# Kernel optimization log

Measured on AMD Instinct MI355X. Metric: run time of the kernel, lower is better.

## Reference

```python
import jax, jax.numpy as jnp
import numpy as np
from jax import lax

EPS = 1e-5

def _conv(x, w, stride=1, pad=0, groups=1):
    return lax.conv_general_dilated(
        x, w, (stride, stride), ((pad, pad), (pad, pad)),
        dimension_numbers=('NCHW', 'OIHW', 'NCHW'),
        feature_group_count=groups)

def _bn(x, gamma, beta):
    # BatchNorm2d, training-mode batch statistics (biased variance)
    mean = jnp.mean(x, axis=(0, 2, 3), keepdims=True)
    var = jnp.var(x, axis=(0, 2, 3), keepdims=True)
    xn = (x - mean) * lax.rsqrt(var + EPS)
    return xn * gamma[None, :, None, None] + beta[None, :, None, None]

def _silu(x):
    return x * jax.nn.sigmoid(x)

def setup_inputs() -> dict:
    key = jax.random.key(0)
    ks = jax.random.split(key, 20)
    B, C, H, W = 16, 128, 128, 128
    L2 = 100
    s = 0.05
    d = {
        'x': jax.random.normal(ks[0], (B, C, H, W), jnp.float32),
        'dce_output': jax.random.normal(ks[1], (B, L2, C), jnp.float32),
        # per-channel 3x3 convs fused as one depthwise conv [C,1,3,3]
        'dw_conv': jax.random.normal(ks[2], (C, 1, 3, 3), jnp.float32) * s,
        'W_dce1': jax.random.normal(ks[3], (L2 * C, C), jnp.float32) * s,
        'b_dce1': jnp.zeros((C,), jnp.float32),
        'W_dce2': jax.random.normal(ks[4], (C, C), jnp.float32) * s,
        'b_dce2': jnp.zeros((C,), jnp.float32),
        'W_sh': jax.random.normal(ks[5], (C, C // 2), jnp.float32) * s,
        'b_sh': jnp.zeros((C // 2,), jnp.float32),
        'W_ex': jax.random.normal(ks[6], (C // 2, C), jnp.float32) * s,
        'b_ex': jnp.zeros((C,), jnp.float32),
        'conv1_w': jax.random.normal(ks[7], (C, C, 3, 3), jnp.float32) * s,
        'bn1_g': jnp.ones((C,), jnp.float32),
        'bn1_b': jnp.zeros((C,), jnp.float32),
        'conv2_w': jax.random.normal(ks[8], (C, C, 1, 1), jnp.float32) * s,
        'bn2_g': jnp.ones((C,), jnp.float32),
        'bn2_b': jnp.zeros((C,), jnp.float32),
        'sc_w': jax.random.normal(ks[9], (C, C, 1, 1), jnp.float32) * s,
        'bnsc_g': jnp.ones((C,), jnp.float32),
        'bnsc_b': jnp.zeros((C,), jnp.float32),
    }
    return d

def reference(x, dce_output, dw_conv, W_dce1, b_dce1, W_dce2, b_dce2,
              W_sh, b_sh, W_ex, b_ex, conv1_w, bn1_g, bn1_b,
              conv2_w, bn2_g, bn2_b, sc_w, bnsc_g, bnsc_b):
    B, C, H, W = x.shape
    stride = 1
    # DCE FFN: Linear -> GELU(exact) -> Linear
    dce_flat = dce_output.reshape(B, -1)
    h = jax.nn.gelu(dce_flat @ W_dce1 + b_dce1, approximate=False)
    dce_features = h @ W_dce2 + b_dce2  # [B, C]
    # per-channel 3x3 conv + global avg pool, fused as depthwise conv
    sp = _conv(x, dw_conv, stride=1, pad=1, groups=C)
    spatial_features = jnp.mean(sp, axis=(2, 3))  # [B, C]
    # SE-style modulation
    m = dce_features * spatial_features
    shrunk = jax.nn.gelu(m @ W_sh + b_sh, approximate=False)
    mod_w = jax.nn.sigmoid(shrunk @ W_ex + b_ex)  # [B, C]
    xm = x * mod_w[:, :, None, None]
    # ResBlock
    bb = _bn(_conv(xm, conv1_w, stride=stride, pad=1), bn1_g, bn1_b)
    bb = _silu(bb)
    bb = _bn(_conv(bb, conv2_w, stride=1, pad=0), bn2_g, bn2_b)
    sc = _bn(_conv(xm, sc_w, stride=stride, pad=0), bnsc_g, bnsc_b)
    return _silu(bb + sc)
```

## Files before the change

### kernel.cpp

```cpp
#include <hip/hip_runtime.h>
#include <hip/hip_bf16.h>

typedef _Float16 f16;
typedef __attribute__((ext_vector_type(8))) _Float16 f16x8;
typedef __attribute__((ext_vector_type(4))) float f32x4;

__device__ __forceinline__ float geluf(float x) {
    return 0.5f * x * (1.0f + erff(x * 0.70710678118654752440f));
}
__device__ __forceinline__ float sigmf(float x) { return 1.0f / (1.0f + __expf(-x)); }

#define NB 16
#define NC 128
#define NH 128
#define NW 128
#define PLANE (NH * NW)
#define NSTAT 262144.0f

__device__ __align__(16) f16 g_Wc[9 * 4 * 128 * 32];
__device__ __align__(16) f16 g_Wsc[4 * 128 * 32];
__device__ __align__(16) f16 g_W2[4 * 128 * 32];
__device__ __align__(16) f16 g_xmT[(size_t)16 * 128 * 4 * 130 * 32];

__global__ __launch_bounds__(256) void k_wprep(const float* __restrict__ c1w,
                                               const float* __restrict__ scw,
                                               const float* __restrict__ c2w) {
    int i = blockIdx.x * 256 + threadIdx.x;
    if (i < 147456) {
        int tap = i / 16384;
        int rem = i - tap * 16384;
        int chunk = rem >> 12;
        int r2 = rem & 4095;
        int co = r2 >> 5;
        int cil = r2 & 31;
        int ci = chunk * 32 + cil;
        g_Wc[i] = (f16)c1w[((size_t)co * 128 + ci) * 9 + tap];
    } else if (i < 163840) {
        int j = i - 147456;
        int chunk = j >> 12;
        int r2 = j & 4095;
        int co = r2 >> 5;
        int cil = r2 & 31;
        g_Wsc[j] = (f16)scw[(size_t)co * 128 + chunk * 32 + cil];
    } else if (i < 180224) {
        int j = i - 163840;
        int chunk = j >> 12;
        int r2 = j & 4095;
        int co = r2 >> 5;
        int cil = j & 31;
        g_W2[j] = (f16)c2w[(size_t)co * 128 + chunk * 32 + cil];
    }
}

__global__ __launch_bounds__(256) void k_dce1(const float* __restrict__ dce,
                                              const float* __restrict__ W1,
                                              const float* __restrict__ b1,
                                              float* __restrict__ out_h) {
    int b = blockIdx.x;
    int t = threadIdx.x;
    int j = t & 127;
    int half = t >> 7;
    __shared__ float sdce[12800];
    __shared__ float sred[256];
    const float* drow = dce + (size_t)b * 12800;
    for (int i = t; i < 3200; i += 256) {
        float4 v = *(const float4*)&drow[i * 4];
        *(float4*)&sdce[i * 4] = v;
    }
    __syncthreads();
    float acc = 0.0f;
    int k0 = half * 6400;
    const float* Wp = W1 + (size_t)k0 * 128 + j;
    for (int k = 0; k < 6400; ++k) acc += sdce[k0 + k] * Wp[(size_t)k * 128];
    sred[t] = acc;
    __syncthreads();
    if (t < 128) {
        float v = sred[t] + sred[t + 128] + b1[j];
        out_h[b * 128 + j] = geluf(v);
    }
}

__global__ __launch_bounds__(128) void k_dce2(const float* __restrict__ h,
                                              const float* __restrict__ W2,
                                              const float* __restrict__ b2,
                                              float* __restrict__ feat) {
    int b = blockIdx.x, j = threadIdx.x;
    __shared__ float sh[128];
    sh[j] = h[b * 128 + j];
    __syncthreads();
    float acc = b2[j];
    for (int k = 0; k < 128; ++k) acc += sh[k] * W2[k * 128 + j];
    feat[b * 128 + j] = acc;
}

__global__ __launch_bounds__(256) void k_spatial(const float* __restrict__ x,
                                                 const float* __restrict__ dw,
                                                 float* __restrict__ spat) {
    int bc = blockIdx.x;
    int t = threadIdx.x;
    const float* p = x + (size_t)bc * PLANE;
    float f = 0, r0 = 0, r1 = 0, c0 = 0, c1 = 0;
    for (int i = t; i < PLANE; i += 256) {
        float v = p[i];
        int row = i >> 7, col = i & 127;
        f += v;
        if (row == 0) r0 += v;
        if (row == 127) r1 += v;
        if (col == 0) c0 += v;
        if (col == 127) c1 += v;
    }
    __shared__ float s[256];
    __shared__ float red[5];
    float vals[5] = {f, r0, r1, c0, c1};
    for (int k = 0; k < 5; ++k) {
        s[t] = vals[k];
        __syncthreads();
        for (int o = 128; o > 0; o >>= 1) {
            if (t < o) s[t] += s[t + o];
            __syncthreads();
        }
        if (t == 0) red[k] = s[0];
        __syncthreads();
    }
    if (t == 0) {
        int c = bc & 127;
        float full = red[0], row0 = red[1], row127 = red[2], col0 = red[3], col127 = red[4];
        float x00 = p[0];
        float x0e = p[127];
        float xe0 = p[127 * 128];
        float xee = p[127 * 128 + 127];
        float acc = 0.0f;
        for (int kh = 0; kh < 3; ++kh)
            for (int kw = 0; kw < 3; ++kw) {
                int dh = kh - 1, dwv = kw - 1;
                float T = full;
                if (dh == -1) T -= row127;
                else if (dh == 1) T -= row0;
                if (dwv == -1) T -= col127;
                else if (dwv == 1) T -= col0;
                if (dh == -1 && dwv == -1) T += xee;
                if (dh == -1 && dwv == 1) T += xe0;
                if (dh == 1 && dwv == -1) T += x0e;
                if (dh == 1 && dwv == 1) T += x00;
                acc += dw[c * 9 + kh * 3 + kw] * T;
            }
        spat[bc] = acc * (1.0f / 16384.0f);
    }
}

__global__ __launch_bounds__(128) void k_mod(const float* __restrict__ feat,
                                             const float* __restrict__ spat,
                                             const float* __restrict__ Wsh,
                                             const float* __restrict__ bsh,
                                             const float* __restrict__ Wex,
                                             const float* __restrict__ bex,
                                             float* __restrict__ mod) {
    int b = blockIdx.x, t = threadIdx.x;
    __shared__ float sm[128], ssh[64];
    sm[t] = feat[b * 128 + t] * spat[b * 128 + t];
    __syncthreads();
    if (t < 64) {
        float acc = bsh[t];
        for (int c = 0; c < 128; ++c) acc += sm[c] * Wsh[c * 64 + t];
        ssh[t] = geluf(acc);
    }
    __syncthreads();
    float acc = bex[t];
    for (int k = 0; k < 64; ++k) acc += ssh[k] * Wex[k * 128 + t];
    mod[b * 128 + t] = sigmf(acc);
}

__global__ __launch_bounds__(256) void k_xprep(const float* __restrict__ x,
                                               const float* __restrict__ mod) {
    int bid = blockIdx.x;
    int h = bid & 127;
    int b = bid >> 7;
    int t = threadIdx.x;
    __shared__ float sx[32][133];

    for (int chunk = 0; chunk < 4; ++chunk) {
        __syncthreads();
#pragma unroll
        for (int it = 0; it < 4; ++it) {
            int ci = it * 8 + (t >> 5);
            int w4 = t & 31;
            int cig = chunk * 32 + ci;
            float4 v = *(const float4*)&x[(((size_t)b * 128 + cig) * 128 + h) * 128 + w4 * 4];
            float m = mod[b * 128 + cig];
            sx[ci][w4 * 4 + 0] = v.x * m;
            sx[ci][w4 * 4 + 1] = v.y * m;
            sx[ci][w4 * 4 + 2] = v.z * m;
            sx[ci][w4 * 4 + 3] = v.w * m;
        }
        __syncthreads();
        f16* dstc = g_xmT + (((size_t)(b * 128 + h)) * 4 + chunk) * 4160;
        for (int g = t; g < 520; g += 256) {
            int s = g >> 2, c8 = g & 3;
            f16x8 o;
            if (s == 0 || s == 129) {
#pragma unroll
                for (int j = 0; j < 8; ++j) o[j] = (f16)0.f;
            } else {
#pragma unroll
                for (int j = 0; j < 8; ++j) o[j] = (f16)sx[c8 * 8 + j][s - 1];
            }
            *(f16x8*)(dstc + s * 32 + c8 * 8) = o;
        }
    }
}

__global__ __launch_bounds__(256, 2) void k_conv1m(float* __restrict__ y1,
                                                   float* __restrict__ stats) {
    int bid = blockIdx.x;
    int h = bid & 127;
    int b = bid >> 7;
    int t = threadIdx.x;
    int lane = t & 63;
    int wv = t >> 6;
    int l15 = lane & 15, lg = lane >> 4;
    int co_half = (wv >> 1) * 64;
    int w_half = (wv & 1) * 64;

    __shared__ f16 xs[3][130][40];

    f32x4 acc[4][4], asc[4][4];
#pragma unroll
    for (int ct = 0; ct < 4; ++ct)
#pragma unroll
        for (int wt = 0; wt < 4; ++wt) {
            acc[ct][wt] = (f32x4){0.f, 0.f, 0.f, 0.f};
            asc[ct][wt] = (f32x4){0.f, 0.f, 0.f, 0.f};
        }

    f16x8 z8;
#pragma unroll
    for (int j = 0; j < 8; ++j) z8[j] = (f16)0.f;

    for (int chunk = 0; chunk < 4; ++chunk) {
        __syncthreads();
        for (int g = t; g < 1560; g += 256) {
            int r = g / 520;
            int q = g - r * 520;
            int s = q >> 2, c8 = q & 3;
            int hr = h + r - 1;
            f16x8 v = z8;
            if ((unsigned)hr < 128u)
                v = *(const f16x8*)(g_xmT + (((size_t)(b * 128 + hr)) * 4 + chunk) * 4160 + s * 32 + c8 * 8);
            *(f16x8*)&xs[r][s][c8 * 8] = v;
        }
        __syncthreads();

#pragma unroll
        for (int tap = 0; tap < 9; ++tap) {
            const int kh = tap / 3, kw = tap - kh * 3;
            f16x8 af[4], bf[4];
#pragma unroll
            for (int ct = 0; ct < 4; ++ct)
                af[ct] = *(const f16x8*)(g_Wc + ((size_t)(tap * 4 + chunk) * 128 + co_half + ct * 16 + l15) * 32 + lg * 8);
#pragma unroll
            for (int wt = 0; wt < 4; ++wt)
                bf[wt] = *(const f16x8*)&xs[kh][w_half + wt * 16 + l15 + kw][lg * 8];
#pragma unroll
            for (int ct = 0; ct < 4; ++ct)
#pragma unroll
                for (int wt = 0; wt < 4; ++wt)
                    acc[ct][wt] = __builtin_amdgcn_mfma_f32_16x16x32_f16(
                        af[ct], bf[wt], acc[ct][wt], 0, 0, 0);

            if (tap == 4) {
                f16x8 sf[4];
#pragma unroll
                for (int ct = 0; ct < 4; ++ct)
                    sf[ct] = *(const f16x8*)(g_Wsc + ((size_t)chunk * 128 + co_half + ct * 16 + l15) * 32 + lg * 8);
#pragma unroll
                for (int ct = 0; ct < 4; ++ct)
#pragma unroll
                    for (int wt = 0; wt < 4; ++wt)
                        asc[ct][wt] = __builtin_amdgcn_mfma_f32_16x16x32_f16(
                            sf[ct], bf[wt], asc[ct][wt], 0, 0, 0);
            }
        }
    }

    float* yb = y1 + (size_t)b * 128 * PLANE + (size_t)h * 128;
#pragma unroll
    for (int ct = 0; ct < 4; ++ct) {
#pragma unroll
        for (int r = 0; r < 4; ++r) {
            int co = co_half + ct * 16 + lg * 4 + r;
            float s = 0, q = 0, ss = 0, qq = 0;
#pragma unroll
            for (int wt = 0; wt < 4; ++wt) {
                float v = acc[ct][wt][r];
                yb[(size_t)co * PLANE + w_half + wt * 16 + l15] = v;
                s += v; q += v * v;
                float u = asc[ct][wt][r];
                ss += u; qq += u * u;
            }
#pragma unroll
            for (int o = 1; o < 16; o <<= 1) {
                s += __shfl_xor(s, o);
                q += __shfl_xor(q, o);
                ss += __shfl_xor(ss, o);
                qq += __shfl_xor(qq, o);
            }
            if (l15 == 0) {
                atomicAdd(&stats[co], s);
                atomicAdd(&stats[128 + co], q);
                atomicAdd(&stats[256 + co], ss);
                atomicAdd(&stats[384 + co], qq);
            }
        }
    }
}

__global__ __launch_bounds__(256) void k_fin1(const float* __restrict__ stats,
                                              const float* __restrict__ g1, const float* __restrict__ be1,
                                              const float* __restrict__ gsc, const float* __restrict__ bsc,
                                              float* __restrict__ coef) {
    int t = threadIdx.x;
    const float inv = 1.0f / NSTAT;
    if (t < 128) {
        float m = stats[t] * inv;
        float v = stats[128 + t] * inv - m * m;
        float a = g1[t] * rsqrtf(v + 1e-5f);
        coef[t] = a;
        coef[128 + t] = be1[t] - m * a;
    } else {
        int c = t - 128;
        float m = stats[256 + c] * inv;
        float v = stats[384 + c] * inv - m * m;
        float a = gsc[c] * rsqrtf(v + 1e-5f);
        coef[256 + c] = a;
        coef[384 + c] = bsc[c] - m * a;
    }
}

__global__ __launch_bounds__(256, 2) void k_conv2m(const float* __restrict__ y1,
                                                   const float* __restrict__ coef,
                                                   float* __restrict__ stats) {
    int bid = blockIdx.x;
    int h = bid & 127;
    int b = bid >> 7;
    int t = threadIdx.x;
    int lane = t & 63;
    int wv = t >> 6;
    int l15 = lane & 15, lg = lane >> 4;
    int co_half = (wv >> 1) * 64;
    int w_half = (wv & 1) * 64;

    __shared__ float sy[32][133];
    __shared__ f16 bbs[128][40];

    f32x4 acc[4][4];
#pragma unroll
    for (int ct = 0; ct < 4; ++ct)
#pragma unroll
        for (int wt = 0; wt < 4; ++wt) acc[ct][wt] = (f32x4){0.f, 0.f, 0.f, 0.f};

    for (int chunk = 0; chunk < 4; ++chunk) {
        __syncthreads();
#pragma unroll
        for (int it = 0; it < 4; ++it) {
            int ci = it * 8 + (t >> 5);
            int w4 = t & 31;
            int cig = chunk * 32 + ci;
            float a = coef[cig], c = coef[128 + cig];
            float4 v = *(const float4*)&y1[(((size_t)b * 128 + cig) * 128 + h) * 128 + w4 * 4];
            float u0 = a * v.x + c; u0 = u0 * sigmf(u0);
            float u1 = a * v.y + c; u1 = u1 * sigmf(u1);
            float u2 = a * v.z + c; u2 = u2 * sigmf(u2);
            float u3 = a * v.w + c; u3 = u3 * sigmf(u3);
            sy[ci][w4 * 4 + 0] = u0;
            sy[ci][w4 * 4 + 1] = u1;
            sy[ci][w4 * 4 + 2] = u2;
            sy[ci][w4 * 4 + 3] = u3;
        }
        __syncthreads();
        for (int g = t; g < 512; g += 256) {
            int s = g >> 2, c8 = g & 3;
            f16x8 o;
#pragma unroll
            for (int j = 0; j < 8; ++j) o[j] = (f16)sy[c8 * 8 + j][s];
            *(f16x8*)&bbs[s][c8 * 8] = o;
        }
        __syncthreads();
        f16x8 af[4], bf[4];
#pragma unroll
        for (int ct = 0; ct < 4; ++ct)
            af[ct] = *(const f16x8*)(g_W2 + ((size_t)chunk * 128 + co_half + ct * 16 + l15) * 32 + lg * 8);
#pragma unroll
        for (int wt = 0; wt < 4; ++wt)
            bf[wt] = *(const f16x8*)&bbs[w_half + wt * 16 + l15][lg * 8];
#pragma unroll
        for (int ct = 0; ct < 4; ++ct)
#pragma unroll
            for (int wt = 0; wt < 4; ++wt)
                acc[ct][wt] = __builtin_amdgcn_mfma_f32_16x16x32_f16(
                    af[ct], bf[wt], acc[ct][wt], 0, 0, 0);
    }

#pragma unroll
    for (int ct = 0; ct < 4; ++ct) {
#pragma unroll
        for (int r = 0; r < 4; ++r) {
            int co = co_half + ct * 16 + lg * 4 + r;
            float s = 0, q = 0;
#pragma unroll
            for (int wt = 0; wt < 4; ++wt) {
                float v = acc[ct][wt][r];
                s += v; q += v * v;
            }
#pragma unroll
            for (int o = 1; o < 16; o <<= 1) {
                s += __shfl_xor(s, o);
                q += __shfl_xor(q, o);
            }
            if (l15 == 0) {
                atomicAdd(&stats[512 + co], s);
                atomicAdd(&stats[640 + co], q);
            }
        }
    }
}

__global__ __launch_bounds__(128) void k_fin2(const float* __restrict__ stats,
                                              const float* __restrict__ g2, const float* __restrict__ be2,
                                              float* __restrict__ coef) {
    int c = threadIdx.x;
    const float inv = 1.0f / NSTAT;
    float m = stats[512 + c] * inv;
    float v = stats[640 + c] * inv - m * m;
    float a = g2[c] * rsqrtf(v + 1e-5f);
    coef[512 + c] = a;
    coef[640 + c] = be2[c] - m * a;
}

__global__ __launch_bounds__(256, 2) void k_final(float* __restrict__ yio,
                                                  const float* __restrict__ coef) {
    int bid = blockIdx.x;
    int h = bid & 127;
    int b = bid >> 7;
    int t = threadIdx.x;
    int lane = t & 63;
    int wv = t >> 6;
    int l15 = lane & 15, lg = lane >> 4;
    int co_half = (wv >> 1) * 64;
    int w_half = (wv & 1) * 64;

    __shared__ float sy[32][133];
    __shared__ f16 bbs[128][40];

    f32x4 acc[4][4], asc[4][4];
#pragma unroll
    for (int ct = 0; ct < 4; ++ct)
#pragma unroll
        for (int wt = 0; wt < 4; ++wt) {
            acc[ct][wt] = (f32x4){0.f, 0.f, 0.f, 0.f};
            asc[ct][wt] = (f32x4){0.f, 0.f, 0.f, 0.f};
        }

    for (int chunk = 0; chunk < 4; ++chunk) {
        __syncthreads();
#pragma unroll
        for (int it = 0; it < 4; ++it) {
            int ci = it * 8 + (t >> 5);
            int w4 = t & 31;
            int cig = chunk * 32 + ci;
            float a = coef[cig], c = coef[128 + cig];
            float4 v = *(const float4*)&yio[(((size_t)b * 128 + cig) * 128 + h) * 128 + w4 * 4];
            float u0 = a * v.x + c; u0 = u0 * sigmf(u0);
            float u1 = a * v.y + c; u1 = u1 * sigmf(u1);
            float u2 = a * v.z + c; u2 = u2 * sigmf(u2);
            float u3 = a * v.w + c; u3 = u3 * sigmf(u3);
            sy[ci][w4 * 4 + 0] = u0;
            sy[ci][w4 * 4 + 1] = u1;
            sy[ci][w4 * 4 + 2] = u2;
            sy[ci][w4 * 4 + 3] = u3;
        }
        __syncthreads();
        for (int g = t; g < 512; g += 256) {
            int s = g >> 2, c8 = g & 3;
            f16x8 o;
#pragma unroll
            for (int j = 0; j < 8; ++j) o[j] = (f16)sy[c8 * 8 + j][s];
            *(f16x8*)&bbs[s][c8 * 8] = o;
        }
        __syncthreads();

        f16x8 af[4], sf[4], bf[4], bx[4];
#pragma unroll
        for (int ct = 0; ct < 4; ++ct) {
            af[ct] = *(const f16x8*)(g_W2 + ((size_t)chunk * 128 + co_half + ct * 16 + l15) * 32 + lg * 8);
            sf[ct] = *(const f16x8*)(g_Wsc + ((size_t)chunk * 128 + co_half + ct * 16 + l15) * 32 + lg * 8);
        }
#pragma unroll
        for (int wt = 0; wt < 4; ++wt) {
            bf[wt] = *(const f16x8*)&bbs[w_half + wt * 16 + l15][lg * 8];
            bx[wt] = *(const f16x8*)(g_xmT + (((size_t)(b * 128 + h)) * 4 + chunk) * 4160
                                     + (w_half + wt * 16 + l15 + 1) * 32 + lg * 8);
        }
#pragma unroll
        for (int ct = 0; ct < 4; ++ct)
#pragma unroll
            for (int wt = 0; wt < 4; ++wt) {
                acc[ct][wt] = __builtin_amdgcn_mfma_f32_16x16x32_f16(
                    af[ct], bf[wt], acc[ct][wt], 0, 0, 0);
                asc[ct][wt] = __builtin_amdgcn_mfma_f32_16x16x32_f16(
                    sf[ct], bx[wt], asc[ct][wt], 0, 0, 0);
            }
    }

#pragma unroll
    for (int ct = 0; ct < 4; ++ct) {
#pragma unroll
        for (int r = 0; r < 4; ++r) {
            int co = co_half + ct * 16 + lg * 4 + r;
            float a2 = coef[512 + co], c2 = coef[640 + co];
            float as = coef[256 + co], cs = coef[384 + co];
#pragma unroll
            for (int wt = 0; wt < 4; ++wt) {
                float v = a2 * acc[ct][wt][r] + c2 + as * asc[ct][wt][r] + cs;
                v = v * sigmf(v);
                yio[(((size_t)b * 128 + co) * 128 + h) * 128 + w_half + wt * 16 + l15] = v;
            }
        }
    }
}

extern "C" void kernel_launch(void* const* d_in, const int* in_sizes, int n_in,
                              void* d_out, int out_size, void* d_ws, size_t ws_size,
                              hipStream_t stream) {
    (void)in_sizes; (void)n_in; (void)out_size; (void)ws_size;
    const float* x    = (const float*)d_in[0];
    const float* dce  = (const float*)d_in[1];
    const float* dwc  = (const float*)d_in[2];
    const float* W1   = (const float*)d_in[3];
    const float* b1   = (const float*)d_in[4];
    const float* W2d  = (const float*)d_in[5];
    const float* b2d  = (const float*)d_in[6];
    const float* Wsh  = (const float*)d_in[7];
    const float* bsh  = (const float*)d_in[8];
    const float* Wex  = (const float*)d_in[9];
    const float* bex  = (const float*)d_in[10];
    const float* c1w  = (const float*)d_in[11];
    const float* g1   = (const float*)d_in[12];
    const float* be1  = (const float*)d_in[13];
    const float* c2w  = (const float*)d_in[14];
    const float* g2   = (const float*)d_in[15];
    const float* be2  = (const float*)d_in[16];
    const float* scw  = (const float*)d_in[17];
    const float* gsc  = (const float*)d_in[18];
    const float* bsc  = (const float*)d_in[19];

    float* F = (float*)d_ws;
    float* dh    = F;
    float* feat  = F + 2048;
    float* spat  = F + 4096;
    float* md    = F + 6144;
    float* stats = F + 8192;
    float* coef  = F + 8960;

    float* y1 = (float*)d_out;

    hipMemsetAsync(stats, 0, 768 * sizeof(float), stream);

    k_wprep<<<704, 256, 0, stream>>>(c1w, scw, c2w);
    k_dce1<<<16, 256, 0, stream>>>(dce, W1, b1, dh);
    k_dce2<<<16, 128, 0, stream>>>(dh, W2d, b2d, feat);
    k_spatial<<<2048, 256, 0, stream>>>(x, dwc, spat);
    k_mod<<<16, 128, 0, stream>>>(feat, spat, Wsh, bsh, Wex, bex, md);
    k_xprep<<<2048, 256, 0, stream>>>(x, md);
    k_conv1m<<<2048, 256, 0, stream>>>(y1, stats);
    k_fin1<<<1, 256, 0, stream>>>(stats, g1, be1, gsc, bsc, coef);
    k_conv2m<<<2048, 256, 0, stream>>>(y1, coef, stats);
    k_fin2<<<1, 128, 0, stream>>>(stats, g2, be2, coef);
    k_final<<<2048, 256, 0, stream>>>(y1, coef);
}
```

Baseline: 1.528 ms.

## Store conv intermediates as fp16 channel-blocked buffers, prefetch conv1 chunks, split DCE GEMV

conv1 now writes its output as fp16 in a channel-blocked transposed layout (g_y1T) instead of fp32 NCHW into the output buffer. The shortcut 1x1 conv moves from conv1 into conv2. conv2 applies BN1+SiLU on the fly, feeds MFMA directly from global memory, and saves the activated tensor (g_bbT), so the final kernel no longer redoes the BN/SiLU/transpose through shared memory. conv1 prefetches the next input-channel chunk into registers while computing and uses a swizzled block order. The DCE first linear is split across 64 blocks with atomics, and the spatial reduction uses wave shuffles. These changes cut fp32 intermediate traffic and shared-memory transposes, at the cost of fp16 rounding of intermediates and more register pressure.

Result: faster. 1.346 ms (-11.9%).

```diff
diff --git a/kernel.cpp b/kernel.cpp
--- a/kernel.cpp
+++ b/kernel.cpp
@@ -3,6 +3,7 @@
 
 typedef _Float16 f16;
 typedef __attribute__((ext_vector_type(8))) _Float16 f16x8;
+typedef __attribute__((ext_vector_type(4))) _Float16 f16x4;
 typedef __attribute__((ext_vector_type(4))) float f32x4;
 
 __device__ __forceinline__ float geluf(float x) {
@@ -21,6 +22,8 @@
 __device__ __align__(16) f16 g_Wsc[4 * 128 * 32];
 __device__ __align__(16) f16 g_W2[4 * 128 * 32];
 __device__ __align__(16) f16 g_xmT[(size_t)16 * 128 * 4 * 130 * 32];
+__device__ __align__(16) f16 g_y1T[(size_t)16 * 128 * 4 * 128 * 32];
+__device__ __align__(16) f16 g_bbT[(size_t)16 * 128 * 4 * 128 * 32];
 
 __global__ __launch_bounds__(256) void k_wprep(const float* __restrict__ c1w,
                                                const float* __restrict__ scw,
@@ -54,39 +57,39 @@
 
 __global__ __launch_bounds__(256) void k_dce1(const float* __restrict__ dce,
                                               const float* __restrict__ W1,
+                                              float* __restrict__ dh) {
+    int ks = blockIdx.x;
+    int kbase = ks * 200;
+    int t = threadIdx.x;
+    __shared__ float sdce[16][256];
+    for (int e = t; e < 4096; e += 256) {
+        int bb = e >> 8, k = e & 255;
+        if (k < 200) sdce[bb][k] = dce[(size_t)bb * 12800 + kbase + k];
+    }
+    __syncthreads();
+    int j = t & 127;
+    int bg = t >> 7;
+    float accs[8];
+#pragma unroll
+    for (int i = 0; i < 8; ++i) accs[i] = 0.0f;
+    for (int k = 0; k < 200; ++k) {
+        float wv = W1[((size_t)(kbase + k)) * 128 + j];
+#pragma unroll
+        for (int bb = 0; bb < 8; ++bb) accs[bb] += sdce[bg * 8 + bb][k] * wv;
+    }
+#pragma unroll
+    for (int bb = 0; bb < 8; ++bb)
+        atomicAdd(&dh[(bg * 8 + bb) * 128 + j], accs[bb]);
+}
+
+__global__ __launch_bounds__(128) void k_dce2(const float* __restrict__ dh,
                                               const float* __restrict__ b1,
-                                              float* __restrict__ out_h) {
-    int b = blockIdx.x;
-    int t = threadIdx.x;
-    int j = t & 127;
-    int half = t >> 7;
-    __shared__ float sdce[12800];
-    __shared__ float sred[256];
-    const float* drow = dce + (size_t)b * 12800;
-    for (int i = t; i < 3200; i += 256) {
-        float4 v = *(const float4*)&drow[i * 4];
-        *(float4*)&sdce[i * 4] = v;
-    }
-    __syncthreads();
-    float acc = 0.0f;
-    int k0 = half * 6400;
-    const float* Wp = W1 + (size_t)k0 * 128 + j;
-    for (int k = 0; k < 6400; ++k) acc += sdce[k0 + k] * Wp[(size_t)k * 128];
-    sred[t] = acc;
-    __syncthreads();
-    if (t < 128) {
-        float v = sred[t] + sred[t + 128] + b1[j];
-        out_h[b * 128 + j] = geluf(v);
-    }
-}
-
-__global__ __launch_bounds__(128) void k_dce2(const float* __restrict__ h,
                                               const float* __restrict__ W2,
                                               const float* __restrict__ b2,
                                               float* __restrict__ feat) {
     int b = blockIdx.x, j = threadIdx.x;
     __shared__ float sh[128];
-    sh[j] = h[b * 128 + j];
+    sh[j] = geluf(dh[b * 128 + j] + b1[j]);
     __syncthreads();
     float acc = b2[j];
     for (int k = 0; k < 128; ++k) acc += sh[k] * W2[k * 128 + j];
@@ -109,22 +112,28 @@
         if (col == 0) c0 += v;
         if (col == 127) c1 += v;
     }
-    __shared__ float s[256];
-    __shared__ float red[5];
-    float vals[5] = {f, r0, r1, c0, c1};
-    for (int k = 0; k < 5; ++k) {
-        s[t] = vals[k];
-        __syncthreads();
-        for (int o = 128; o > 0; o >>= 1) {
-            if (t < o) s[t] += s[t + o];
-            __syncthreads();
-        }
-        if (t == 0) red[k] = s[0];
-        __syncthreads();
-    }
+#pragma unroll
+    for (int o = 1; o < 64; o <<= 1) {
+        f  += __shfl_xor(f, o);
+        r0 += __shfl_xor(r0, o);
+        r1 += __shfl_xor(r1, o);
+        c0 += __shfl_xor(c0, o);
+        c1 += __shfl_xor(c1, o);
+    }
+    __shared__ float wr[4][5];
+    int wid = t >> 6;
+    if ((t & 63) == 0) {
+        wr[wid][0] = f; wr[wid][1] = r0; wr[wid][2] = r1; wr[wid][3] = c0; wr[wid][4] = c1;
+    }
+    __syncthreads();
     if (t == 0) {
+        float full = 0, row0 = 0, row127 = 0, col0 = 0, col127 = 0;
+#pragma unroll
+        for (int w = 0; w < 4; ++w) {
+            full += wr[w][0]; row0 += wr[w][1]; row127 += wr[w][2];
+            col0 += wr[w][3]; col127 += wr[w][4];
+        }
         int c = bc & 127;
-        float full = red[0], row0 = red[1], row127 = red[2], col0 = red[3], col127 = red[4];
         float x00 = p[0];
         float x0e = p[127];
         float xe0 = p[127 * 128];
@@ -132,16 +141,16 @@
         float acc = 0.0f;
         for (int kh = 0; kh < 3; ++kh)
             for (int kw = 0; kw < 3; ++kw) {
-                int dh = kh - 1, dwv = kw - 1;
+                int dh_ = kh - 1, dwv = kw - 1;
                 float T = full;
-                if (dh == -1) T -= row127;
-                else if (dh == 1) T -= row0;
+                if (dh_ == -1) T -= row127;
+                else if (dh_ == 1) T -= row0;
                 if (dwv == -1) T -= col127;
                 else if (dwv == 1) T -= col0;
-                if (dh == -1 && dwv == -1) T += xee;
-                if (dh == -1 && dwv == 1) T += xe0;
-                if (dh == 1 && dwv == -1) T += x0e;
-                if (dh == 1 && dwv == 1) T += x00;
+                if (dh_ == -1 && dwv == -1) T += xee;
+                if (dh_ == -1 && dwv == 1) T += xe0;
+                if (dh_ == 1 && dwv == -1) T += x0e;
+                if (dh_ == 1 && dwv == 1) T += x00;
                 acc += dw[c * 9 + kh * 3 + kw] * T;
             }
         spat[bc] = acc * (1.0f / 16384.0f);
@@ -209,11 +218,11 @@
     }
 }
 
-__global__ __launch_bounds__(256, 2) void k_conv1m(float* __restrict__ y1,
-                                                   float* __restrict__ stats) {
-    int bid = blockIdx.x;
-    int h = bid & 127;
-    int b = bid >> 7;
+__global__ __launch_bounds__(256, 2) void k_conv1m(float* __restrict__ stats) {
+    int orig = blockIdx.x;
+    int sw = (orig & 7) * 256 + (orig >> 3);
+    int h = sw & 127;
+    int b = sw >> 7;
     int t = threadIdx.x;
     int lane = t & 63;
     int wv = t >> 6;
@@ -223,32 +232,58 @@
 
     __shared__ f16 xs[3][130][40];
 
-    f32x4 acc[4][4], asc[4][4];
+    f32x4 acc[4][4];
 #pragma unroll
     for (int ct = 0; ct < 4; ++ct)
 #pragma unroll
-        for (int wt = 0; wt < 4; ++wt) {
-            acc[ct][wt] = (f32x4){0.f, 0.f, 0.f, 0.f};
-            asc[ct][wt] = (f32x4){0.f, 0.f, 0.f, 0.f};
-        }
+        for (int wt = 0; wt < 4; ++wt) acc[ct][wt] = (f32x4){0.f, 0.f, 0.f, 0.f};
 
     f16x8 z8;
 #pragma unroll
     for (int j = 0; j < 8; ++j) z8[j] = (f16)0.f;
 
-    for (int chunk = 0; chunk < 4; ++chunk) {
-        __syncthreads();
-        for (int g = t; g < 1560; g += 256) {
+    f16x8 st[7];
+
+#pragma unroll
+    for (int i = 0; i < 7; ++i) {
+        int g = t + i * 256;
+        if (g < 1560) {
             int r = g / 520;
             int q = g - r * 520;
             int s = q >> 2, c8 = q & 3;
             int hr = h + r - 1;
-            f16x8 v = z8;
+            st[i] = z8;
             if ((unsigned)hr < 128u)
-                v = *(const f16x8*)(g_xmT + (((size_t)(b * 128 + hr)) * 4 + chunk) * 4160 + s * 32 + c8 * 8);
-            *(f16x8*)&xs[r][s][c8 * 8] = v;
-        }
-        __syncthreads();
+                st[i] = *(const f16x8*)(g_xmT + (((size_t)(b * 128 + hr)) * 4 + 0) * 4160 + s * 32 + c8 * 8);
+        }
+    }
+#pragma unroll
+    for (int i = 0; i < 7; ++i) {
+        int g = t + i * 256;
+        if (g < 1560) {
+            int r = g / 520;
+            int q = g - r * 520;
+            *(f16x8*)&xs[r][q >> 2][(q & 3) * 8] = st[i];
+        }
+    }
+    __syncthreads();
+
+    for (int chunk = 0; chunk < 4; ++chunk) {
+        if (chunk < 3) {
+#pragma unroll
+            for (int i = 0; i < 7; ++i) {
+                int g = t + i * 256;
+                if (g < 1560) {
+                    int r = g / 520;
+                    int q = g - r * 520;
+                    int s = q >> 2, c8 = q & 3;
+                    int hr = h + r - 1;
+                    st[i] = z8;
+                    if ((unsigned)hr < 128u)
+                        st[i] = *(const f16x8*)(g_xmT + (((size_t)(b * 128 + hr)) * 4 + chunk + 1) * 4160 + s * 32 + c8 * 8);
+                }
+            }
+        }
 
 #pragma unroll
         for (int tap = 0; tap < 9; ++tap) {
@@ -266,23 +301,136 @@
                 for (int wt = 0; wt < 4; ++wt)
                     acc[ct][wt] = __builtin_amdgcn_mfma_f32_16x16x32_f16(
                         af[ct], bf[wt], acc[ct][wt], 0, 0, 0);
-
-            if (tap == 4) {
-                f16x8 sf[4];
-#pragma unroll
-                for (int ct = 0; ct < 4; ++ct)
-                    sf[ct] = *(const f16x8*)(g_Wsc + ((size_t)chunk * 128 + co_half + ct * 16 + l15) * 32 + lg * 8);
-#pragma unroll
-                for (int ct = 0; ct < 4; ++ct)
-#pragma unroll
-                    for (int wt = 0; wt < 4; ++wt)
-                        asc[ct][wt] = __builtin_amdgcn_mfma_f32_16x16x32_f16(
-                            sf[ct], bf[wt], asc[ct][wt], 0, 0, 0);
-            }
-        }
-    }
-
-    float* yb = y1 + (size_t)b * 128 * PLANE + (size_t)h * 128;
+        }
+
+        __syncthreads();
+        if (chunk < 3) {
+#pragma unroll
+            for (int i = 0; i < 7; ++i) {
+                int g = t + i * 256;
+                if (g < 1560) {
+                    int r = g / 520;
+                    int q = g - r * 520;
+                    *(f16x8*)&xs[r][q >> 2][(q & 3) * 8] = st[i];
+                }
+            }
+            __syncthreads();
+        }
+    }
+
+#pragma unroll
+    for (int ct = 0; ct < 4; ++ct) {
+        int cog = (wv >> 1) * 2 + (ct >> 1);
+        int col = (ct & 1) * 16 + lg * 4;
+#pragma unroll
+        for (int wt = 0; wt < 4; ++wt) {
+            int w = w_half + wt * 16 + l15;
+            f16x4 pk;
+            pk[0] = (f16)acc[ct][wt][0];
+            pk[1] = (f16)acc[ct][wt][1];
+            pk[2] = (f16)acc[ct][wt][2];
+            pk[3] = (f16)acc[ct][wt][3];
+            *(f16x4*)(g_y1T + ((((size_t)(b * 128 + h)) * 4 + cog) * 128 + w) * 32 + col) = pk;
+        }
+#pragma unroll
+        for (int r = 0; r < 4; ++r) {
+            int co = co_half + ct * 16 + lg * 4 + r;
+            float s = 0, q = 0;
+#pragma unroll
+            for (int wt = 0; wt < 4; ++wt) {
+                float v = acc[ct][wt][r];
+                s += v; q += v * v;
+            }
+#pragma unroll
+            for (int o = 1; o < 16; o <<= 1) {
+                s += __shfl_xor(s, o);
+                q += __shfl_xor(q, o);
+            }
+            if (l15 == 0) {
+                atomicAdd(&stats[co], s);
+                atomicAdd(&stats[128 + co], q);
+            }
+        }
+    }
+}
+
+__global__ __launch_bounds__(128) void k_fin1(const float* __restrict__ stats,
+                                              const float* __restrict__ g1, const float* __restrict__ be1,
+                                              float* __restrict__ coef) {
+    int t = threadIdx.x;
+    const float inv = 1.0f / NSTAT;
+    float m = stats[t] * inv;
+    float v = stats[128 + t] * inv - m * m;
+    float a = g1[t] * rsqrtf(v + 1e-5f);
+    coef[t] = a;
+    coef[128 + t] = be1[t] - m * a;
+}
+
+__global__ __launch_bounds__(256, 2) void k_conv2m(const float* __restrict__ coef,
+                                                   float* __restrict__ stats) {
+    int bid = blockIdx.x;
+    int h = bid & 127;
+    int b = bid >> 7;
+    int t = threadIdx.x;
+    int lane = t & 63;
+    int wv = t >> 6;
+    int l15 = lane & 15, lg = lane >> 4;
+    int co_half = (wv >> 1) * 64;
+    int w_half = (wv & 1) * 64;
+
+    f32x4 acc[4][4], asc[4][4];
+#pragma unroll
+    for (int ct = 0; ct < 4; ++ct)
+#pragma unroll
+        for (int wt = 0; wt < 4; ++wt) {
+            acc[ct][wt] = (f32x4){0.f, 0.f, 0.f, 0.f};
+            asc[ct][wt] = (f32x4){0.f, 0.f, 0.f, 0.f};
+        }
+
+    for (int chunk = 0; chunk < 4; ++chunk) {
+        float ca[8], cc[8];
+#pragma unroll
+        for (int j = 0; j < 8; ++j) {
+            int ci = chunk * 32 + lg * 8 + j;
+            ca[j] = coef[ci];
+            cc[j] = coef[128 + ci];
+        }
+        f16x8 bfr[4], bx[4];
+#pragma unroll
+        for (int wt = 0; wt < 4; ++wt) {
+            int w = w_half + wt * 16 + l15;
+            f16x8 raw = *(const f16x8*)(g_y1T + ((((size_t)(b * 128 + h)) * 4 + chunk) * 128 + w) * 32 + lg * 8);
+#pragma unroll
+            for (int j = 0; j < 8; ++j) {
+                float v = ca[j] * (float)raw[j] + cc[j];
+                bfr[wt][j] = (f16)(v * sigmf(v));
+            }
+            bx[wt] = *(const f16x8*)(g_xmT + (((size_t)(b * 128 + h)) * 4 + chunk) * 4160 + (w + 1) * 32 + lg * 8);
+        }
+        if (wv < 2) {
+#pragma unroll
+            for (int wt = 0; wt < 4; ++wt) {
+                int w = w_half + wt * 16 + l15;
+                *(f16x8*)(g_bbT + ((((size_t)(b * 128 + h)) * 4 + chunk) * 128 + w) * 32 + lg * 8) = bfr[wt];
+            }
+        }
+        f16x8 af[4], sf[4];
+#pragma unroll
+        for (int ct = 0; ct < 4; ++ct) {
+            af[ct] = *(const f16x8*)(g_W2 + ((size_t)chunk * 128 + co_half + ct * 16 + l15) * 32 + lg * 8);
+            sf[ct] = *(const f16x8*)(g_Wsc + ((size_t)chunk * 128 + co_half + ct * 16 + l15) * 32 + lg * 8);
+        }
+#pragma unroll
+        for (int ct = 0; ct < 4; ++ct)
+#pragma unroll
+            for (int wt = 0; wt < 4; ++wt) {
+                acc[ct][wt] = __builtin_amdgcn_mfma_f32_16x16x32_f16(
+                    af[ct], bfr[wt], acc[ct][wt], 0, 0, 0);
+                asc[ct][wt] = __builtin_amdgcn_mfma_f32_16x16x32_f16(
+                    sf[ct], bx[wt], asc[ct][wt], 0, 0, 0);
+            }
+    }
+
 #pragma unroll
     for (int ct = 0; ct < 4; ++ct) {
 #pragma unroll
@@ -292,7 +440,6 @@
 #pragma unroll
             for (int wt = 0; wt < 4; ++wt) {
                 float v = acc[ct][wt][r];
-                yb[(size_t)co * PLANE + w_half + wt * 16 + l15] = v;
                 s += v; q += v * v;
                 float u = asc[ct][wt][r];
                 ss += u; qq += u * u;
@@ -305,8 +452,8 @@
                 qq += __shfl_xor(qq, o);
             }
             if (l15 == 0) {
-                atomicAdd(&stats[co], s);
-                atomicAdd(&stats[128 + co], q);
+                atomicAdd(&stats[512 + co], s);
+                atomicAdd(&stats[640 + co], q);
                 atomicAdd(&stats[256 + co], ss);
                 atomicAdd(&stats[384 + co], qq);
             }
@@ -314,18 +461,18 @@
     }
 }
 
-__global__ __launch_bounds__(256) void k_fin1(const float* __restrict__ stats,
-                                              const float* __restrict__ g1, const float* __restrict__ be1,
+__global__ __launch_bounds__(256) void k_fin2(const float* __restrict__ stats,
+                                              const float* __restrict__ g2, const float* __restrict__ be2,
                                               const float* __restrict__ gsc, const float* __restrict__ bsc,
                                               float* __restrict__ coef) {
     int t = threadIdx.x;
     const float inv = 1.0f / NSTAT;
     if (t < 128) {
-        float m = stats[t] * inv;
-        float v = stats[128 + t] * inv - m * m;
-        float a = g1[t] * rsqrtf(v + 1e-5f);
-        coef[t] = a;
-        coef[128 + t] = be1[t] - m * a;
+        float m = stats[512 + t] * inv;
+        float v = stats[640 + t] * inv - m * m;
+        float a = g2[t] * rsqrtf(v + 1e-5f);
+        coef[512 + t] = a;
+        coef[640 + t] = be2[t] - m * a;
     } else {
         int c = t - 128;
         float m = stats[256 + c] * inv;
@@ -336,9 +483,8 @@
     }
 }
 
-__global__ __launch_bounds__(256, 2) void k_conv2m(const float* __restrict__ y1,
-                                                   const float* __restrict__ coef,
-                                                   float* __restrict__ stats) {
+__global__ __launch_bounds__(256, 2) void k_final(float* __restrict__ out,
+                                                  const float* __restrict__ coef) {
     int bid = blockIdx.x;
     int h = bid & 127;
     int b = bid >> 7;
@@ -349,108 +495,6 @@
     int co_half = (wv >> 1) * 64;
     int w_half = (wv & 1) * 64;
 
-    __shared__ float sy[32][133];
-    __shared__ f16 bbs[128][40];
-
-    f32x4 acc[4][4];
-#pragma unroll
-    for (int ct = 0; ct < 4; ++ct)
-#pragma unroll
-        for (int wt = 0; wt < 4; ++wt) acc[ct][wt] = (f32x4){0.f, 0.f, 0.f, 0.f};
-
-    for (int chunk = 0; chunk < 4; ++chunk) {
-        __syncthreads();
-#pragma unroll
-        for (int it = 0; it < 4; ++it) {
-            int ci = it * 8 + (t >> 5);
-            int w4 = t & 31;
-            int cig = chunk * 32 + ci;
-            float a = coef[cig], c = coef[128 + cig];
-            float4 v = *(const float4*)&y1[(((size_t)b * 128 + cig) * 128 + h) * 128 + w4 * 4];
-            float u0 = a * v.x + c; u0 = u0 * sigmf(u0);
-            float u1 = a * v.y + c; u1 = u1 * sigmf(u1);
-            float u2 = a * v.z + c; u2 = u2 * sigmf(u2);
-            float u3 = a * v.w + c; u3 = u3 * sigmf(u3);
-            sy[ci][w4 * 4 + 0] = u0;
-            sy[ci][w4 * 4 + 1] = u1;
-            sy[ci][w4 * 4 + 2] = u2;
-            sy[ci][w4 * 4 + 3] = u3;
-        }
-        __syncthreads();
-        for (int g = t; g < 512; g += 256) {
-            int s = g >> 2, c8 = g & 3;
-            f16x8 o;
-#pragma unroll
-            for (int j = 0; j < 8; ++j) o[j] = (f16)sy[c8 * 8 + j][s];
-            *(f16x8*)&bbs[s][c8 * 8] = o;
-        }
-        __syncthreads();
-        f16x8 af[4], bf[4];
-#pragma unroll
-        for (int ct = 0; ct < 4; ++ct)
-            af[ct] = *(const f16x8*)(g_W2 + ((size_t)chunk * 128 + co_half + ct * 16 + l15) * 32 + lg * 8);
-#pragma unroll
-        for (int wt = 0; wt < 4; ++wt)
-            bf[wt] = *(const f16x8*)&bbs[w_half + wt * 16 + l15][lg * 8];
-#pragma unroll
-        for (int ct = 0; ct < 4; ++ct)
-#pragma unroll
-            for (int wt = 0; wt < 4; ++wt)
-                acc[ct][wt] = __builtin_amdgcn_mfma_f32_16x16x32_f16(
-                    af[ct], bf[wt], acc[ct][wt], 0, 0, 0);
-    }
-
-#pragma unroll
-    for (int ct = 0; ct < 4; ++ct) {
-#pragma unroll
-        for (int r = 0; r < 4; ++r) {
-            int co = co_half + ct * 16 + lg * 4 + r;
-            float s = 0, q = 0;
-#pragma unroll
-            for (int wt = 0; wt < 4; ++wt) {
-                float v = acc[ct][wt][r];
-                s += v; q += v * v;
-            }
-#pragma unroll
-            for (int o = 1; o < 16; o <<= 1) {
-                s += __shfl_xor(s, o);
-                q += __shfl_xor(q, o);
-            }
-            if (l15 == 0) {
-                atomicAdd(&stats[512 + co], s);
-                atomicAdd(&stats[640 + co], q);
-            }
-        }
-    }
-}
-
-__global__ __launch_bounds__(128) void k_fin2(const float* __restrict__ stats,
-                                              const float* __restrict__ g2, const float* __restrict__ be2,
-                                              float* __restrict__ coef) {
-    int c = threadIdx.x;
-    const float inv = 1.0f / NSTAT;
-    float m = stats[512 + c] * inv;
-    float v = stats[640 + c] * inv - m * m;
-    float a = g2[c] * rsqrtf(v + 1e-5f);
-    coef[512 + c] = a;
-    coef[640 + c] = be2[c] - m * a;
-}
-
-__global__ __launch_bounds__(256, 2) void k_final(float* __restrict__ yio,
-                                                  const float* __restrict__ coef) {
-    int bid = blockIdx.x;
-    int h = bid & 127;
-    int b = bid >> 7;
-    int t = threadIdx.x;
-    int lane = t & 63;
-    int wv = t >> 6;
-    int l15 = lane & 15, lg = lane >> 4;
-    int co_half = (wv >> 1) * 64;
-    int w_half = (wv & 1) * 64;
-
-    __shared__ float sy[32][133];
-    __shared__ f16 bbs[128][40];
-
     f32x4 acc[4][4], asc[4][4];
 #pragma unroll
     for (int ct = 0; ct < 4; ++ct)
@@ -461,44 +505,17 @@
         }
 
     for (int chunk = 0; chunk < 4; ++chunk) {
-        __syncthreads();
-#pragma unroll
-        for (int it = 0; it < 4; ++it) {
-            int ci = it * 8 + (t >> 5);
-            int w4 = t & 31;
-            int cig = chunk * 32 + ci;
-            float a = coef[cig], c = coef[128 + cig];
-            float4 v = *(const float4*)&yio[(((size_t)b * 128 + cig) * 128 + h) * 128 + w4 * 4];
-            float u0 = a * v.x + c; u0 = u0 * sigmf(u0);
-            float u1 = a * v.y + c; u1 = u1 * sigmf(u1);
-            float u2 = a * v.z + c; u2 = u2 * sigmf(u2);
-            float u3 = a * v.w + c; u3 = u3 * sigmf(u3);
-            sy[ci][w4 * 4 + 0] = u0;
-            sy[ci][w4 * 4 + 1] = u1;
-            sy[ci][w4 * 4 + 2] = u2;
-            sy[ci][w4 * 4 + 3] = u3;
-        }
-        __syncthreads();
-        for (int g = t; g < 512; g += 256) {
-            int s = g >> 2, c8 = g & 3;
-            f16x8 o;
-#pragma unroll
-            for (int j = 0; j < 8; ++j) o[j] = (f16)sy[c8 * 8 + j][s];
-            *(f16x8*)&bbs[s][c8 * 8] = o;
-        }
-        __syncthreads();
-
-        f16x8 af[4], sf[4], bf[4], bx[4];
+        f16x8 bf[4], bx[4], af[4], sf[4];
+#pragma unroll
+        for (int wt = 0; wt < 4; ++wt) {
+            int w = w_half + wt * 16 + l15;
+            bf[wt] = *(const f16x8*)(g_bbT + ((((size_t)(b * 128 + h)) * 4 + chunk) * 128 + w) * 32 + lg * 8);
+            bx[wt] = *(const f16x8*)(g_xmT + (((size_t)(b * 128 + h)) * 4 + chunk) * 4160 + (w + 1) * 32 + lg * 8);
+        }
 #pragma unroll
         for (int ct = 0; ct < 4; ++ct) {
             af[ct] = *(const f16x8*)(g_W2 + ((size_t)chunk * 128 + co_half + ct * 16 + l15) * 32 + lg * 8);
             sf[ct] = *(const f16x8*)(g_Wsc + ((size_t)chunk * 128 + co_half + ct * 16 + l15) * 32 + lg * 8);
-        }
-#pragma unroll
-        for (int wt = 0; wt < 4; ++wt) {
-            bf[wt] = *(const f16x8*)&bbs[w_half + wt * 16 + l15][lg * 8];
-            bx[wt] = *(const f16x8*)(g_xmT + (((size_t)(b * 128 + h)) * 4 + chunk) * 4160
-                                     + (w_half + wt * 16 + l15 + 1) * 32 + lg * 8);
         }
 #pragma unroll
         for (int ct = 0; ct < 4; ++ct)
@@ -522,7 +539,7 @@
             for (int wt = 0; wt < 4; ++wt) {
                 float v = a2 * acc[ct][wt][r] + c2 + as * asc[ct][wt][r] + cs;
                 v = v * sigmf(v);
-                yio[(((size_t)b * 128 + co) * 128 + h) * 128 + w_half + wt * 16 + l15] = v;
+                out[(((size_t)b * 128 + co) * 128 + h) * 128 + w_half + wt * 16 + l15] = v;
             }
         }
     }
@@ -555,25 +572,25 @@
 
     float* F = (float*)d_ws;
     float* dh    = F;
-    float* feat  = F + 2048;
-    float* spat  = F + 4096;
-    float* md    = F + 6144;
-    float* stats = F + 8192;
-    float* coef  = F + 8960;
-
-    float* y1 = (float*)d_out;
-
-    hipMemsetAsync(stats, 0, 768 * sizeof(float), stream);
+    float* stats = F + 2048;
+    float* coef  = F + 2816;
+    float* feat  = F + 3584;
+    float* spat  = F + 5632;
+    float* md    = F + 7680;
+
+    float* out = (float*)d_out;
+
+    hipMemsetAsync(F, 0, (2048 + 768) * sizeof(float), stream);
 
     k_wprep<<<704, 256, 0, stream>>>(c1w, scw, c2w);
-    k_dce1<<<16, 256, 0, stream>>>(dce, W1, b1, dh);
-    k_dce2<<<16, 128, 0, stream>>>(dh, W2d, b2d, feat);
+    k_dce1<<<64, 256, 0, stream>>>(dce, W1, dh);
+    k_dce2<<<16, 128, 0, stream>>>(dh, b1, W2d, b2d, feat);
     k_spatial<<<2048, 256, 0, stream>>>(x, dwc, spat);
     k_mod<<<16, 128, 0, stream>>>(feat, spat, Wsh, bsh, Wex, bex, md);
     k_xprep<<<2048, 256, 0, stream>>>(x, md);
-    k_conv1m<<<2048, 256, 0, stream>>>(y1, stats);
-    k_fin1<<<1, 256, 0, stream>>>(stats, g1, be1, gsc, bsc, coef);
-    k_conv2m<<<2048, 256, 0, stream>>>(y1, coef, stats);
-    k_fin2<<<1, 128, 0, stream>>>(stats, g2, be2, coef);
-    k_final<<<2048, 256, 0, stream>>>(y1, coef);
-}
+    k_conv1m<<<2048, 256, 0, stream>>>(stats);
+    k_fin1<<<1, 128, 0, stream>>>(stats, g1, be1, coef);
+    k_conv2m<<<2048, 256, 0, stream>>>(coef, stats);
+    k_fin2<<<1, 256, 0, stream>>>(stats, g2, be2, gsc, bsc, coef);
+    k_final<<<2048, 256, 0, stream>>>(out, coef);
+}
```
